# Performance work log

Hardware: AMD Instinct MI355X
Metric: run time of the kernel (lower is better)

## Reference

```python
import jax, jax.numpy as jnp
import numpy as np

N = 50000      # nodes
E = 800000     # edges (before self loops)
H = 4          # heads
C = 32         # hidden_channels per head
HC = H * C     # 128
L = 3          # num_layers - 2 conv blocks
G = 128        # graphs in batch
OUT = 10       # out_channels
VOCAB = 100
EPS = 1e-5


def setup_inputs() -> dict:
    key = jax.random.key(0)
    ks = jax.random.split(key, 16)
    s = 0.1
    return {
        "x_idx": jax.random.randint(ks[0], (N,), 0, VOCAB),
        "edge_index": jax.random.randint(ks[1], (2, E), 0, N),
        "batch": jnp.sort(jax.random.randint(ks[2], (N,), 0, G)),
        "embed": jax.random.normal(ks[3], (VOCAB, HC), jnp.float32) * s,
        "bn_gamma": jnp.ones((L, HC), jnp.float32),
        "bn_beta": jnp.zeros((L, HC), jnp.float32),
        "lin_W": jax.random.normal(ks[4], (L, C, HC), jnp.float32) * s,   # maps HC -> C (hidden)
        "lin_b": jnp.zeros((L, C), jnp.float32),
        "gat_W": jax.random.normal(ks[5], (L, HC, C), jnp.float32) * s,   # maps C -> H*C
        "att_src": jax.random.normal(ks[6], (L, H, C), jnp.float32) * s,
        "att_dst": jax.random.normal(ks[7], (L, H, C), jnp.float32) * s,
        "gat_b": jnp.zeros((L, HC), jnp.float32),
        "readout_W": jax.random.normal(ks[8], (OUT, HC), jnp.float32) * s,
        "readout_b": jnp.zeros((OUT,), jnp.float32),
    }


def _segment_softmax(logits, seg, num_segments):
    # logits: [E, H], seg: [E]
    m = jax.ops.segment_max(logits, seg, num_segments=num_segments)
    m = jnp.where(jnp.isfinite(m), m, 0.0)
    e = jnp.exp(logits - m[seg])
    z = jax.ops.segment_sum(e, seg, num_segments=num_segments)
    return e / (z[seg] + 1e-16)


def _forward(x_idx, edge_index, batch, embed, bn_gamma, bn_beta, lin_W, lin_b,
             gat_W, att_src, att_dst, gat_b, readout_W, readout_b):
    x = embed[x_idx]                                   # [N, HC]
    loops = jnp.arange(N)
    src = jnp.concatenate([edge_index[0], loops])      # add_self_loops=True
    dst = jnp.concatenate([edge_index[1], loops])
    for l in range(L):
        # BatchNorm1d (batch statistics)
        mean = jnp.mean(x, axis=0)
        var = jnp.var(x, axis=0)
        x = bn_gamma[l] * (x - mean) * jax.lax.rsqrt(var + EPS) + bn_beta[l]
        # Linear(HC -> C) + relu; dropout = identity (eval)
        x = jax.nn.relu(x @ lin_W[l].T + lin_b[l])      # [N, C]
        # GATConv(C -> C, heads=H, concat)
        h = (x @ gat_W[l].T).reshape(N, H, C)           # [N, H, C]
        a_src = jnp.sum(h * att_src[l], axis=-1)        # [N, H]
        a_dst = jnp.sum(h * att_dst[l], axis=-1)        # [N, H]
        logits = jax.nn.leaky_relu(a_src[src] + a_dst[dst], 0.2)  # [E+N, H]
        alpha = _segment_softmax(logits, dst, N)        # softmax over in-edges of each dst
        msg = h[src] * alpha[:, :, None]                # [E+N, H, C]
        x = jax.ops.segment_sum(msg, dst, num_segments=N).reshape(N, HC) + gat_b[l]
    x = x @ readout_W.T + readout_b                     # [N, OUT]
    return jax.ops.segment_sum(x, batch, num_segments=G)  # [G, OUT]


def reference(x_idx, edge_index, batch, embed, bn_gamma, bn_beta, lin_W, lin_b,
              gat_W, att_src, att_dst, gat_b, readout_W, readout_b):
    return _forward(x_idx, edge_index, batch, embed, bn_gamma, bn_beta, lin_W, lin_b,
                    gat_W, att_src, att_dst, gat_b, readout_W, readout_b)
```

## Files before the change

### kernel.cpp

```cpp
#include <hip/hip_runtime.h>

constexpr int NN   = 50000;
constexpr int NE   = 800000;
constexpr int NHD  = 4;
constexpr int CC   = 32;
constexpr int HCC  = 128;
constexpr int NL   = 3;
constexpr int NG   = 128;
constexpr int NOUT = 10;
constexpr float BN_EPS = 1e-5f;

constexpr int X2S = 67;
constexpr int YS = 33;
constexpr int NSLOT = 64;
constexpr int SCB = (NN + 1023) / 1024;
constexpr int NBUK = (NN + 127) / 128;
constexpr int EB  = 8192;

__device__ inline unsigned f2bf_pack(float a, float b) {
    unsigned ua = __float_as_uint(a); ua += 0x7FFFu + ((ua >> 16) & 1u);
    unsigned ub = __float_as_uint(b); ub += 0x7FFFu + ((ub >> 16) & 1u);
    return (ua >> 16) | (ub & 0xFFFF0000u);
}
__device__ inline float bf_lo(unsigned p) { return __uint_as_float(p << 16); }
__device__ inline float bf_hi(unsigned p) { return __uint_as_float(p & 0xFFFF0000u); }

__global__ __launch_bounds__(256) void k_embed_hist(const int* __restrict__ idx,
                                                    const float* __restrict__ embed,
                                                    float* __restrict__ x,
                                                    float* __restrict__ stats,
                                                    const int* __restrict__ ei,
                                                    int* __restrict__ deg) {
    int tid = threadIdx.x;
    int e = blockIdx.x * 256 + tid;
    if (e < NE) atomicAdd(&deg[ei[NE + e]], 1);

    int i0 = blockIdx.x * 256 + tid;
    int stride = gridDim.x * 256;
    float s = 0.f, q = 0.f;
    for (int i = i0; i < NN * HCC; i += stride) {
        float v = embed[idx[i >> 7] * HCC + (i & 127)];
        x[i] = v; s += v; q += v * v;
    }
    __shared__ float ssum[256], ssq[256];
    ssum[tid] = s; ssq[tid] = q;
    __syncthreads();
    int slot = blockIdx.x & (NSLOT - 1);
    if (tid < HCC) {
        atomicAdd(&stats[slot * 256 + tid],       ssum[tid] + ssum[tid + HCC]);
        atomicAdd(&stats[slot * 256 + HCC + tid], ssq[tid]  + ssq[tid + HCC]);
    }
}

__global__ __launch_bounds__(256) void k_scan1(const int* __restrict__ deg,
                                               int* __restrict__ rowptr,
                                               int* __restrict__ part) {
    __shared__ int sh[256];
    int b = blockIdx.x, t = threadIdx.x;
    int base = b * 1024 + t * 4;
    int v0 = (base     < NN) ? deg[base]     : 0;
    int v1 = (base + 1 < NN) ? deg[base + 1] : 0;
    int v2 = (base + 2 < NN) ? deg[base + 2] : 0;
    int v3 = (base + 3 < NN) ? deg[base + 3] : 0;
    int s = v0 + v1 + v2 + v3;
    sh[t] = s;
    __syncthreads();
#pragma unroll
    for (int off = 1; off < 256; off <<= 1) {
        int u = (t >= off) ? sh[t - off] : 0;
        __syncthreads();
        sh[t] += u;
        __syncthreads();
    }
    if (t == 255) part[b] = sh[255];
    int p = sh[t] - s;
    if (base     < NN) rowptr[base]     = p; p += v0;
    if (base + 1 < NN) rowptr[base + 1] = p; p += v1;
    if (base + 2 < NN) rowptr[base + 2] = p; p += v2;
    if (base + 3 < NN) rowptr[base + 3] = p;
}

__global__ void k_scan2(int* __restrict__ part, int* __restrict__ rowptr) {
    if (threadIdx.x == 0) {
        int run = 0;
        for (int i = 0; i < SCB; i++) { int v = part[i]; part[i] = run; run += v; }
        rowptr[NN] = run;
    }
}

__global__ __launch_bounds__(256) void k_scan3(int* __restrict__ rowptr,
                                               const int* __restrict__ part,
                                               int* __restrict__ bcnt) {
    int b = blockIdx.x, t = threadIdx.x;
    int off = part[b];
    int base = b * 1024 + t * 4;
#pragma unroll
    for (int k = 0; k < 4; k++) {
        int ix = base + k;
        if (ix < NN) {
            int v = rowptr[ix] + off;
            rowptr[ix] = v;
            if ((ix & 127) == 0) bcnt[ix >> 7] = v;
        }
    }
}

__global__ __launch_bounds__(256) void k_bin(const int* __restrict__ ei,
                                             int* __restrict__ bcnt,
                                             unsigned* __restrict__ e_src) {
    __shared__ int hist[NBUK], base[NBUK];
    int b = blockIdx.x, t = threadIdx.x;
    int e0 = b * EB;
    int nE = min(EB, NE - e0);

    for (int i = t; i < NBUK; i += 256) hist[i] = 0;
    __syncthreads();
    for (int i = t; i < nE; i += 256)
        atomicAdd(&hist[ei[NE + e0 + i] >> 7], 1);
    __syncthreads();
    for (int i = t; i < NBUK; i += 256) {
        int c = hist[i];
        if (c) base[i] = atomicAdd(&bcnt[i], c);
        hist[i] = 0;
    }
    __syncthreads();
    for (int i = t; i < nE; i += 256) {
        int e = e0 + i;
        int d = ei[NE + e];
        int s = ei[e];
        int bk = d >> 7;
        int pos = base[bk] + atomicAdd(&hist[bk], 1);
        e_src[pos] = (unsigned)s | ((unsigned)(d & 127) << 17);
    }
}

__global__ __launch_bounds__(256) void k_place(const int* __restrict__ rowptr,
                                               unsigned* __restrict__ e_src) {
    __shared__ int lrp[129];
    __shared__ int cnt[128];
    int b = blockIdx.x, t = threadIdx.x;
    int d0 = b * 128;
    if (t < 128) {
        int ix = d0 + t;
        lrp[t] = (ix <= NN) ? rowptr[ix] : NE;
        cnt[t] = 0;
    }
    if (t == 0) lrp[128] = rowptr[min(d0 + 128, NN)];
    __syncthreads();
    int rS = lrp[0], rE = lrp[128];
    int n = rE - rS;
    unsigned pk[14];
#pragma unroll
    for (int k = 0; k < 14; k++) {
        int i = t + k * 256;
        if (i < n) pk[k] = e_src[rS + i];
    }
    __syncthreads();
#pragma unroll
    for (int k = 0; k < 14; k++) {
        int i = t + k * 256;
        if (i < n) {
            unsigned p = pk[k];
            int dl = p >> 17;
            int pos = lrp[dl] + atomicAdd(&cnt[dl], 1);
            e_src[pos] = p & 0x1FFFFu;
        }
    }
}

__global__ __launch_bounds__(256) void k_fused(const float* __restrict__ x,
                                               const float* __restrict__ stats,
                                               const float* __restrict__ gamma,
                                               const float* __restrict__ beta,
                                               const float* __restrict__ W1,
                                               const float* __restrict__ b1,
                                               const float* __restrict__ W2,
                                               const float* __restrict__ aS,
                                               const float* __restrict__ aD,
                                               unsigned* __restrict__ h,
                                               float* __restrict__ asrc,
                                               float* __restrict__ adst) {
    __shared__ unsigned xb2[64 * X2S];
    __shared__ float yt[64 * YS];
    __shared__ float ssl[256];
    int tid = threadIdx.x;
    int node0 = blockIdx.x * 64;
    int nNodes = min(64, NN - node0);

    if (tid < 128) {
        float s = 0.f, q = 0.f;
        for (int sl = 0; sl < NSLOT; sl++) {
            s += stats[sl * 256 + tid];
            q += stats[sl * 256 + HCC + tid];
        }
        float mean = s * (1.0f / NN);
        float var  = q * (1.0f / NN) - mean * mean;
        float sc   = gamma[tid] * rsqrtf(var + BN_EPS);
        ssl[tid]       = sc;
        ssl[HCC + tid] = beta[tid] - mean * sc;
    }
    __syncthreads();

    {
        int cS = (tid * 4) & 127;
        float4 scv = *(const float4*)&ssl[cS];
        float4 shv = *(const float4*)&ssl[HCC + cS];
        for (int f4 = tid; f4 < nNodes * 32; f4 += 256) {
            int f = f4 * 4; int n = f >> 7; int c = f & 127;
            float4 xv = *(const float4*)(x + (size_t)(node0 + n) * HCC + c);
            float v0 = xv.x * scv.x + shv.x;
            float v1 = xv.y * scv.y + shv.y;
            float v2 = xv.z * scv.z + shv.z;
            float v3 = xv.w * scv.w + shv.w;
            unsigned* dst = &xb2[n * X2S + (c >> 1)];
            dst[0] = f2bf_pack(v0, v1);
            dst[1] = f2bf_pack(v2, v3);
        }
    }
    __syncthreads();

    int lane = tid & 63;
    int wv = __builtin_amdgcn_readfirstlane(tid >> 6);
    int n = lane;

    {
        int j0 = wv * 8;
        const float* w1p = W1 + j0 * 128;
        float acc[8];
#pragma unroll
        for (int k = 0; k < 8; k++) acc[k] = b1[j0 + k];
        if (n < nNodes) {
            for (int cb = 0; cb < 128; cb += 4) {
                unsigned p0 = xb2[n * X2S + (cb >> 1)];
                unsigned p1 = xb2[n * X2S + (cb >> 1) + 1];
                float xv0 = bf_lo(p0), xv1 = bf_hi(p0);
                float xv2 = bf_lo(p1), xv3 = bf_hi(p1);
#pragma unroll
                for (int k = 0; k < 8; k++) {
                    float4 w = *(const float4*)&w1p[k * 128 + cb];
                    acc[k] += xv0 * w.x + xv1 * w.y + xv2 * w.z + xv3 * w.w;
                }
            }
#pragma unroll
            for (int k = 0; k < 8; k++) yt[n * YS + j0 + k] = fmaxf(acc[k], 0.f);
        }
    }
    __syncthreads();

    if (n < nNodes) {
        int k0 = wv * 32, hd = wv;
        const float* w2p = W2 + k0 * 32;
        const float* aSp = aS + hd * 32;
        const float* aDp = aD + hd * 32;
        float yreg[32];
#pragma unroll
        for (int j = 0; j < 32; j++) yreg[j] = yt[n * YS + j];
        float sa = 0.f, da = 0.f;
        unsigned* hrow = h + (size_t)(node0 + n) * 64;
        for (int kb = 0; kb < 32; kb += 8) {
            float acck[8];
#pragma unroll
            for (int kk = 0; kk < 8; kk++) acck[kk] = 0.f;
#pragma unroll
            for (int j = 0; j < 32; j += 4) {
#pragma unroll
                for (int kk = 0; kk < 8; kk++) {
                    float4 w = *(const float4*)&w2p[(kb + kk) * 32 + j];
                    acck[kk] += yreg[j] * w.x + yreg[j + 1] * w.y +
                                yreg[j + 2] * w.z + yreg[j + 3] * w.w;
                }
            }
#pragma unroll
            for (int kk = 0; kk < 8; kk++) {
                sa += acck[kk] * aSp[kb + kk];
                da += acck[kk] * aDp[kb + kk];
            }
            uint4 pk;
            pk.x = f2bf_pack(acck[0], acck[1]);
            pk.y = f2bf_pack(acck[2], acck[3]);
            pk.z = f2bf_pack(acck[4], acck[5]);
            pk.w = f2bf_pack(acck[6], acck[7]);
            *(uint4*)(hrow + ((kb) >> 1) + (k0 >> 1)) = pk;
        }
        asrc[(node0 + n) * 4 + hd] = sa;
        adst[(node0 + n) * 4 + hd] = da;
    }
}

__global__ __launch_bounds__(256) void k_agg(const int* __restrict__ rowptr,
                                             const int* __restrict__ e_src,
                                             const float* __restrict__ asrc,
                                             const float* __restrict__ adst,
                                             const unsigned* __restrict__ h,
                                             const float* __restrict__ gat_b,
                                             float* __restrict__ xo,
                                             float* __restrict__ stats,
                                             int do_stats) {
    int tid = threadIdx.x, lane = tid & 63, wv = tid >> 6;
    int g  = lane >> 4;
    int li = lane & 15;
    int hd = li >> 2;
    int d  = blockIdx.x * 16 + wv * 4 + g;

    float4 bA = *(const float4*)(gat_b + li * 8);
    float4 bB = *(const float4*)(gat_b + li * 8 + 4);

    int begin = rowptr[d];
    int end   = rowptr[d + 1];
    float adv = adst[d * 4 + hd];
    float asl = asrc[d * 4 + hd];
    uint4 hs  = *(const uint4*)(h + (size_t)d * 64 + li * 4);

    float acc[8];
#pragma unroll
    for (int k = 0; k < 8; k++) acc[k] = 0.f;
    float ws = 0.f;

    int s[4];
    if (begin < end) {
#pragma unroll
        for (int t = 0; t < 4; t++) s[t] = e_src[min(begin + t, end - 1)];
    }

    for (int j = begin; j < end; j += 4) {
        uint4 hv[4];
#pragma unroll
        for (int t = 0; t < 4; t++) hv[t] = *(const uint4*)(h + (size_t)s[t] * 64 + li * 4);
        float av[4];
#pragma unroll
        for (int t = 0; t < 4; t++) av[t] = asrc[s[t] * 4 + hd];
        int jn = j + 4;
        int sn[4];
#pragma unroll
        for (int t = 0; t < 4; t++) sn[t] = s[t];
        if (jn < end) {
#pragma unroll
            for (int t = 0; t < 4; t++) sn[t] = e_src[min(jn + t, end - 1)];
        }
        float w[4];
#pragma unroll
        for (int t = 0; t < 4; t++) {
            float l = av[t] + adv; l = l > 0.f ? l : 0.2f * l;
            w[t] = (j + t < end) ? __expf(l) : 0.f;
        }
#pragma unroll
        for (int t = 0; t < 4; t++) {
            acc[0] += w[t] * bf_lo(hv[t].x); acc[1] += w[t] * bf_hi(hv[t].x);
            acc[2] += w[t] * bf_lo(hv[t].y); acc[3] += w[t] * bf_hi(hv[t].y);
            acc[4] += w[t] * bf_lo(hv[t].z); acc[5] += w[t] * bf_hi(hv[t].z);
            acc[6] += w[t] * bf_lo(hv[t].w); acc[7] += w[t] * bf_hi(hv[t].w);
            ws += w[t];
        }
#pragma unroll
        for (int t = 0; t < 4; t++) s[t] = sn[t];
    }

    {
        float l = asl + adv; l = l > 0.f ? l : 0.2f * l;
        float w = __expf(l);
        acc[0] += w * bf_lo(hs.x); acc[1] += w * bf_hi(hs.x);
        acc[2] += w * bf_lo(hs.y); acc[3] += w * bf_hi(hs.y);
        acc[4] += w * bf_lo(hs.z); acc[5] += w * bf_hi(hs.z);
        acc[6] += w * bf_lo(hs.w); acc[7] += w * bf_hi(hs.w);
        ws += w;
    }

    float inv = 1.0f / (ws + 1e-16f);
    float o[8];
    o[0] = acc[0] * inv + bA.x; o[1] = acc[1] * inv + bA.y;
    o[2] = acc[2] * inv + bA.z; o[3] = acc[3] * inv + bA.w;
    o[4] = acc[4] * inv + bB.x; o[5] = acc[5] * inv + bB.y;
    o[6] = acc[6] * inv + bB.z; o[7] = acc[7] * inv + bB.w;
    float* orow = xo + (size_t)d * HCC + li * 8;
    *(float4*)orow       = make_float4(o[0], o[1], o[2], o[3]);
    *(float4*)(orow + 4) = make_float4(o[4], o[5], o[6], o[7]);

    if (!do_stats) return;
    __shared__ float redS[16 * 128], redQ[16 * 128];
    int r = wv * 4 + g;
#pragma unroll
    for (int k = 0; k < 8; k++) {
        redS[r * 128 + li * 8 + k] = o[k];
        redQ[r * 128 + li * 8 + k] = o[k] * o[k];
    }
    __syncthreads();
    int slot = blockIdx.x & (NSLOT - 1);
    if (tid < 128) {
        float v = 0.f;
#pragma unroll
        for (int rr = 0; rr < 16; rr++) v += redS[rr * 128 + tid];
        atomicAdd(&stats[slot * 256 + tid], v);
    } else {
        int c = tid - 128;
        float v = 0.f;
#pragma unroll
        for (int rr = 0; rr < 16; rr++) v += redQ[rr * 128 + c];
        atomicAdd(&stats[slot * 256 + HCC + c], v);
    }
}

__global__ __launch_bounds__(256) void k_pool(const float* __restrict__ x,
                                              const int* __restrict__ batch,
                                              float* __restrict__ gsum,
                                              float* __restrict__ gcnt) {
    int nb = blockIdx.x * 64, t = threadIdx.x;
    int c = t & 127, half = t >> 7;
    float s = 0.f, cnt = 0.f;
    int curg = -1;
    for (int k = half; k < 64; k += 2) {
        int n = nb + k;
        if (n >= NN) break;
        int g = batch[n];
        if (g != curg) {
            if (curg >= 0) {
                atomicAdd(&gsum[curg * HCC + c], s);
                if (c == 0) atomicAdd(&gcnt[curg], cnt);
            }
            curg = g; s = 0.f; cnt = 0.f;
        }
        s += x[(size_t)n * HCC + c];
        cnt += 1.f;
    }
    if (curg >= 0) {
        atomicAdd(&gsum[curg * HCC + c], s);
        if (c == 0) atomicAdd(&gcnt[curg], cnt);
    }
}

__global__ __launch_bounds__(128) void k_out(const float* __restrict__ gsum,
                                             const float* __restrict__ gcnt,
                                             const float* __restrict__ W,
                                             const float* __restrict__ bb,
                                             float* __restrict__ out) {
    __shared__ float v[128];
    int g = blockIdx.x, t = threadIdx.x;
    v[t] = gsum[g * HCC + t];
    __syncthreads();
    if (t < NOUT) {
        float acc = gcnt[g] * bb[t];
        const float* wr = W + t * HCC;
        for (int c = 0; c < HCC; c++) acc += v[c] * wr[c];
        out[g * NOUT + t] = acc;
    }
}

extern "C" void kernel_launch(void* const* d_in, const int* in_sizes, int n_in,
                              void* d_out, int out_size, void* d_ws, size_t ws_size,
                              hipStream_t stream) {
    const int*   x_idx = (const int*)d_in[0];
    const int*   ei    = (const int*)d_in[1];
    const int*   batch = (const int*)d_in[2];
    const float* embed = (const float*)d_in[3];
    const float* bn_g  = (const float*)d_in[4];
    const float* bn_b  = (const float*)d_in[5];
    const float* lin_W = (const float*)d_in[6];
    const float* lin_b = (const float*)d_in[7];
    const float* gat_W = (const float*)d_in[8];
    const float* att_s = (const float*)d_in[9];
    const float* att_d = (const float*)d_in[10];
    const float* gat_b = (const float*)d_in[11];
    const float* ro_W  = (const float*)d_in[12];
    const float* ro_b  = (const float*)d_in[13];
    float* out = (float*)d_out;

    const size_t STG = (size_t)NSLOT * 256;
    float*    x     = (float*)d_ws;
    unsigned* h     = (unsigned*)(x + (size_t)NN * HCC);
    float*    asrc  = (float*)(h + (size_t)NN * 64);
    float*    adst  = asrc + (size_t)NN * NHD;
    float*    stats = adst + (size_t)NN * NHD;
    float*    gsum  = stats + 3 * STG;
    float*    gcnt  = gsum + (size_t)NG * HCC;
    int*      deg    = (int*)(gcnt + NG);
    int*      rowptr = deg + NN;
    unsigned* e_src  = (unsigned*)(rowptr + NN + 1);
    int*      bcnt   = (int*)(e_src + NE);
    int*      part   = bcnt + NBUK;

    hipMemsetAsync(stats, 0,
                   (3 * STG + (size_t)NG * HCC + NG) * sizeof(float) + NN * sizeof(int),
                   stream);

    k_embed_hist<<<(NE + 255) / 256, 256, 0, stream>>>(x_idx, embed, x, stats, ei, deg);
    k_scan1<<<SCB, 256, 0, stream>>>(deg, rowptr, part);
    k_scan2<<<1, 64, 0, stream>>>(part, rowptr);
    k_scan3<<<SCB, 256, 0, stream>>>(rowptr, part, bcnt);
    k_bin<<<(NE + EB - 1) / EB, 256, 0, stream>>>(ei, bcnt, e_src);
    k_place<<<NBUK, 256, 0, stream>>>(rowptr, e_src);

    for (int l = 0; l < NL; ++l) {
        k_fused<<<(NN + 63) / 64, 256, 0, stream>>>(x, stats + l * STG,
                                                    bn_g + l * HCC, bn_b + l * HCC,
                                                    lin_W + l * CC * HCC, lin_b + l * CC,
                                                    gat_W + l * HCC * CC,
                                                    att_s + l * NHD * CC,
                                                    att_d + l * NHD * CC,
                                                    h, asrc, adst);
        k_agg<<<NN / 16, 256, 0, stream>>>(rowptr, (const int*)e_src, asrc, adst, h,
                                           gat_b + l * HCC, x,
                                           stats + (l + 1) * STG,
                                           (l < NL - 1) ? 1 : 0);
    }

    k_pool<<<(NN + 63) / 64, 256, 0, stream>>>(x, batch, gsum, gcnt);
    k_out<<<NG, 128, 0, stream>>>(gsum, gcnt, ro_W, ro_b, out);
}
```

Before: 390.6 us.

## Build CSR from bucket histogram instead of per-node degree scan

Replaces the per-node degree atomics and the three-pass global scan with a per-bucket histogram (128 destinations per bucket) and a single-block scan over buckets. Per-node row pointers are then computed inside k_place from a local shared-memory histogram and scan of the bucket's edges. The embedding/stats kernel now runs on a fixed 512-block grid, no longer sized by edge count. This removes 800K global atomics on the degree array and two scan launches, at the cost of an extra pass reading the destination indices and an in-block scan in k_place.

```diff
diff --git a/kernel.cpp b/kernel.cpp
--- a/kernel.cpp
+++ b/kernel.cpp
@@ -13,7 +13,6 @@
 constexpr int X2S = 67;
 constexpr int YS = 33;
 constexpr int NSLOT = 64;
-constexpr int SCB = (NN + 1023) / 1024;
 constexpr int NBUK = (NN + 127) / 128;
 constexpr int EB  = 8192;
 
@@ -25,16 +24,11 @@
 __device__ inline float bf_lo(unsigned p) { return __uint_as_float(p << 16); }
 __device__ inline float bf_hi(unsigned p) { return __uint_as_float(p & 0xFFFF0000u); }
 
-__global__ __launch_bounds__(256) void k_embed_hist(const int* __restrict__ idx,
-                                                    const float* __restrict__ embed,
-                                                    float* __restrict__ x,
-                                                    float* __restrict__ stats,
-                                                    const int* __restrict__ ei,
-                                                    int* __restrict__ deg) {
+__global__ __launch_bounds__(256) void k_embed_stats(const int* __restrict__ idx,
+                                                     const float* __restrict__ embed,
+                                                     float* __restrict__ x,
+                                                     float* __restrict__ stats) {
     int tid = threadIdx.x;
-    int e = blockIdx.x * 256 + tid;
-    if (e < NE) atomicAdd(&deg[ei[NE + e]], 1);
-
     int i0 = blockIdx.x * 256 + tid;
     int stride = gridDim.x * 256;
     float s = 0.f, q = 0.f;
@@ -52,57 +46,42 @@
     }
 }
 
-__global__ __launch_bounds__(256) void k_scan1(const int* __restrict__ deg,
-                                               int* __restrict__ rowptr,
-                                               int* __restrict__ part) {
-    __shared__ int sh[256];
+__global__ __launch_bounds__(256) void k_bhist(const int* __restrict__ ei,
+                                               int* __restrict__ bkcnt) {
+    __shared__ int hist[NBUK];
     int b = blockIdx.x, t = threadIdx.x;
-    int base = b * 1024 + t * 4;
-    int v0 = (base     < NN) ? deg[base]     : 0;
-    int v1 = (base + 1 < NN) ? deg[base + 1] : 0;
-    int v2 = (base + 2 < NN) ? deg[base + 2] : 0;
-    int v3 = (base + 3 < NN) ? deg[base + 3] : 0;
-    int s = v0 + v1 + v2 + v3;
-    sh[t] = s;
-    __syncthreads();
-#pragma unroll
-    for (int off = 1; off < 256; off <<= 1) {
-        int u = (t >= off) ? sh[t - off] : 0;
+    int e0 = b * EB, nE = min(EB, NE - e0);
+    for (int i = t; i < NBUK; i += 256) hist[i] = 0;
+    __syncthreads();
+    for (int i = t; i < nE; i += 256)
+        atomicAdd(&hist[ei[NE + e0 + i] >> 7], 1);
+    __syncthreads();
+    for (int i = t; i < NBUK; i += 256)
+        if (hist[i]) atomicAdd(&bkcnt[i], hist[i]);
+}
+
+__global__ __launch_bounds__(512) void k_bscan(const int* __restrict__ bkcnt,
+                                               int* __restrict__ bbase,
+                                               int* __restrict__ bcnt,
+                                               int* __restrict__ rowptr) {
+    __shared__ int sc[512];
+    int t = threadIdx.x;
+    int v = (t < NBUK) ? bkcnt[t] : 0;
+    sc[t] = v;
+    __syncthreads();
+#pragma unroll
+    for (int off = 1; off < 512; off <<= 1) {
+        int u = (t >= off) ? sc[t - off] : 0;
         __syncthreads();
-        sh[t] += u;
+        sc[t] += u;
         __syncthreads();
     }
-    if (t == 255) part[b] = sh[255];
-    int p = sh[t] - s;
-    if (base     < NN) rowptr[base]     = p; p += v0;
-    if (base + 1 < NN) rowptr[base + 1] = p; p += v1;
-    if (base + 2 < NN) rowptr[base + 2] = p; p += v2;
-    if (base + 3 < NN) rowptr[base + 3] = p;
-}
-
-__global__ void k_scan2(int* __restrict__ part, int* __restrict__ rowptr) {
-    if (threadIdx.x == 0) {
-        int run = 0;
-        for (int i = 0; i < SCB; i++) { int v = part[i]; part[i] = run; run += v; }
-        rowptr[NN] = run;
-    }
-}
-
-__global__ __launch_bounds__(256) void k_scan3(int* __restrict__ rowptr,
-                                               const int* __restrict__ part,
-                                               int* __restrict__ bcnt) {
-    int b = blockIdx.x, t = threadIdx.x;
-    int off = part[b];
-    int base = b * 1024 + t * 4;
-#pragma unroll
-    for (int k = 0; k < 4; k++) {
-        int ix = base + k;
-        if (ix < NN) {
-            int v = rowptr[ix] + off;
-            rowptr[ix] = v;
-            if ((ix & 127) == 0) bcnt[ix >> 7] = v;
-        }
-    }
+    if (t < NBUK) {
+        int excl = sc[t] - v;
+        bbase[t] = excl;
+        bcnt[t]  = excl;
+    }
+    if (t == 0) rowptr[NN] = NE;
 }
 
 __global__ __launch_bounds__(256) void k_bin(const int* __restrict__ ei,
@@ -134,26 +113,41 @@
     }
 }
 
-__global__ __launch_bounds__(256) void k_place(const int* __restrict__ rowptr,
-                                               unsigned* __restrict__ e_src) {
-    __shared__ int lrp[129];
-    __shared__ int cnt[128];
+__global__ __launch_bounds__(256) void k_place(const int* __restrict__ bbase,
+                                               unsigned* __restrict__ e_src,
+                                               int* __restrict__ rowptr) {
+    __shared__ int lcnt[128], sc[128], lrp[128], cnt[128];
     int b = blockIdx.x, t = threadIdx.x;
     int d0 = b * 128;
-    if (t < 128) {
-        int ix = d0 + t;
-        lrp[t] = (ix <= NN) ? rowptr[ix] : NE;
-        cnt[t] = 0;
-    }
-    if (t == 0) lrp[128] = rowptr[min(d0 + 128, NN)];
-    __syncthreads();
-    int rS = lrp[0], rE = lrp[128];
+    int rS = bbase[b];
+    int rE = (b + 1 < NBUK) ? bbase[b + 1] : NE;
     int n = rE - rS;
+    if (t < 128) { lcnt[t] = 0; cnt[t] = 0; }
+    __syncthreads();
     unsigned pk[14];
 #pragma unroll
     for (int k = 0; k < 14; k++) {
         int i = t + k * 256;
-        if (i < n) pk[k] = e_src[rS + i];
+        if (i < n) {
+            pk[k] = e_src[rS + i];
+            atomicAdd(&lcnt[pk[k] >> 17], 1);
+        }
+    }
+    __syncthreads();
+    if (t < 128) sc[t] = lcnt[t];
+    __syncthreads();
+#pragma unroll
+    for (int off = 1; off < 128; off <<= 1) {
+        int u = (t < 128 && t >= off) ? sc[t - off] : 0;
+        __syncthreads();
+        if (t < 128) sc[t] += u;
+        __syncthreads();
+    }
+    if (t < 128) {
+        int start = rS + sc[t] - lcnt[t];
+        lrp[t] = start;
+        int d = d0 + t;
+        if (d < NN) rowptr[d] = start;
     }
     __syncthreads();
 #pragma unroll
@@ -471,22 +465,21 @@
     float*    stats = adst + (size_t)NN * NHD;
     float*    gsum  = stats + 3 * STG;
     float*    gcnt  = gsum + (size_t)NG * HCC;
-    int*      deg    = (int*)(gcnt + NG);
-    int*      rowptr = deg + NN;
+    int*      bkcnt  = (int*)(gcnt + NG);
+    int*      bbase  = bkcnt + NBUK;
+    int*      bcnt   = bbase + NBUK;
+    int*      rowptr = bcnt + NBUK;
     unsigned* e_src  = (unsigned*)(rowptr + NN + 1);
-    int*      bcnt   = (int*)(e_src + NE);
-    int*      part   = bcnt + NBUK;
 
     hipMemsetAsync(stats, 0,
-                   (3 * STG + (size_t)NG * HCC + NG) * sizeof(float) + NN * sizeof(int),
+                   (3 * STG + (size_t)NG * HCC + NG) * sizeof(float) + NBUK * sizeof(int),
                    stream);
 
-    k_embed_hist<<<(NE + 255) / 256, 256, 0, stream>>>(x_idx, embed, x, stats, ei, deg);
-    k_scan1<<<SCB, 256, 0, stream>>>(deg, rowptr, part);
-    k_scan2<<<1, 64, 0, stream>>>(part, rowptr);
-    k_scan3<<<SCB, 256, 0, stream>>>(rowptr, part, bcnt);
+    k_embed_stats<<<512, 256, 0, stream>>>(x_idx, embed, x, stats);
+    k_bhist<<<(NE + EB - 1) / EB, 256, 0, stream>>>(ei, bkcnt);
+    k_bscan<<<1, 512, 0, stream>>>(bkcnt, bbase, bcnt, rowptr);
     k_bin<<<(NE + EB - 1) / EB, 256, 0, stream>>>(ei, bcnt, e_src);
-    k_place<<<NBUK, 256, 0, stream>>>(rowptr, e_src);
+    k_place<<<NBUK, 256, 0, stream>>>(bbase, e_src, rowptr);
 
     for (int l = 0; l < NL; ++l) {
         k_fused<<<(NN + 63) / 64, 256, 0, stream>>>(x, stats + l * STG,
```

New measurement: 373.2 us. -4.5%, faster.
